# Kernel optimization log

Hardware: AMD Instinct MI355X
Metric: run time of the kernel (lower is better)

Reference implementation:

```python
import jax, jax.numpy as jnp
import numpy as np

N_NODES = 50000
N_EDGES = 800000
IN_FEATS = 128
HEADS = 8
OUT_FEATS = 32
NEG_SLOPE = 0.2


def setup_inputs() -> dict:
    key = jax.random.key(0)
    k_feat, k_w, k_al, k_ar, k_src, k_dst = jax.random.split(key, 6)
    feat = jax.random.normal(k_feat, (N_NODES, IN_FEATS), dtype=jnp.float32)
    W_fc = jax.random.normal(k_w, (HEADS * OUT_FEATS, IN_FEATS), dtype=jnp.float32) * 0.1
    attn_l = jax.random.normal(k_al, (1, HEADS, OUT_FEATS), dtype=jnp.float32) * 0.1
    attn_r = jax.random.normal(k_ar, (1, HEADS, OUT_FEATS), dtype=jnp.float32) * 0.1
    src = jax.random.randint(k_src, (N_EDGES,), 0, N_NODES, dtype=jnp.int32)
    dst = jax.random.randint(k_dst, (N_EDGES,), 0, N_NODES, dtype=jnp.int32)
    return {"feat": feat, "W_fc": W_fc, "attn_l": attn_l, "attn_r": attn_r,
            "src": src, "dst": dst}


def reference(feat, W_fc, attn_l, attn_r, src, dst):
    N = feat.shape[0]
    H, D = attn_l.shape[1], attn_l.shape[2]
    # fc projection: [N, H, D]
    feat_hd = (feat @ W_fc.T).reshape(N, H, D)
    # per-node left/right attention logits: [N, H]
    el = (feat_hd * attn_l).sum(-1)
    er = (feat_hd * attn_r).sum(-1)
    # u_add_v gather -> per-edge score [E, H], then leaky relu
    e = el[src] + er[dst]
    e = jnp.where(e > 0, e, NEG_SLOPE * e)
    # edge softmax: segment softmax over edges grouped by dst node
    m = jax.ops.segment_max(e, dst, num_segments=N)        # [N, H]
    a = jnp.exp(e - m[dst])                                # [E, H]
    z = jax.ops.segment_sum(a, dst, num_segments=N)        # [N, H]
    a = a / z[dst]
    # u_mul_e + sum: weighted scatter-aggregation -> [N, H, D]
    msg = feat_hd[src] * a[:, :, None]                     # [E, H, D]
    out = jax.ops.segment_sum(msg, dst, num_segments=N)
    return out
```

## Files before the change

### kernel.cpp

```cpp
#include <hip/hip_runtime.h>

#define N_NODES_C 50000
#define N_EDGES_C 800000
#define IN_FEATS_C 128
#define HEADS_C 8
#define HD_C 256
#define NEG_SLOPE_C 0.2f
#define SCAN_NBLK 49
#define LDT 136

#define GEMM_BLOCKS 782
#define DEG_BLOCKS 242
#define K1_GRID (GEMM_BLOCKS + DEG_BLOCKS)

typedef __attribute__((ext_vector_type(8))) short bf16x8;
typedef __attribute__((ext_vector_type(4))) float floatx4;

__device__ inline unsigned short f2bf(float f) {
  unsigned int u = __float_as_uint(f);
  unsigned int r = (u + 0x7FFFu + ((u >> 16) & 1u)) >> 16;
  return (unsigned short)r;
}
__device__ inline float bf2f(unsigned short s) {
  unsigned int u = ((unsigned int)s) << 16;
  return __uint_as_float(u);
}

__device__ inline void boff_scan(const int* __restrict__ bsum, int* sboff) {
  int t = threadIdx.x;
  if (t < 64) {
    int own = (t < SCAN_NBLK) ? bsum[t] : 0;
    int v = own;
#pragma unroll
    for (int off = 1; off < 64; off <<= 1) {
      int u = __shfl_up(v, off);
      if (t >= off) v += u;
    }
    sboff[t] = v - own;
  }
  __syncthreads();
}

__global__ __launch_bounds__(256) void front_kernel(
    const float* __restrict__ feat, const float* __restrict__ W,
    const float* __restrict__ attn_l, const float* __restrict__ attn_r,
    const int* __restrict__ dst,
    unsigned short* __restrict__ feat_hd_bf,
    float* __restrict__ el, float* __restrict__ er,
    int* __restrict__ deg) {
  __shared__ __align__(16) unsigned short sA[128 * LDT];
  __shared__ float sAttnL[128];
  __shared__ float sAttnR[128];
  const int bid = blockIdx.x;
  const int t = threadIdx.x;

  if (bid >= GEMM_BLOCKS) {
    for (int e = (bid - GEMM_BLOCKS) * 256 + t; e < N_EDGES_C;
         e += DEG_BLOCKS * 256)
      atomicAdd(&deg[dst[e]], 1);
    return;
  }

  const int nt = bid & 1;
  const int mt = bid >> 1;
  const int m0 = mt * 128;
  const int n0 = nt * 128;

  if (t < 128) {
    sAttnL[t] = attn_l[n0 + t];
    sAttnR[t] = attn_r[n0 + t];
  }
#pragma unroll
  for (int i = 0; i < 16; ++i) {
    int idx = t + i * 256;
    int row = idx >> 5;
    int c4 = idx & 31;
    int gn = m0 + row;
    float4 v = (gn < N_NODES_C)
                   ? *(const float4*)&feat[(size_t)gn * IN_FEATS_C + c4 * 4]
                   : make_float4(0.f, 0.f, 0.f, 0.f);
    ushort4 b;
    b.x = f2bf(v.x); b.y = f2bf(v.y); b.z = f2bf(v.z); b.w = f2bf(v.w);
    *(ushort4*)&sA[row * LDT + c4 * 4] = b;
  }
  __syncthreads();

  const int wid = t >> 6;
  const int lane = t & 63;
  const int quad = lane >> 4;
  const int l16 = lane & 15;
  const int wm = (wid & 1) * 64;
  const int wn = (wid >> 1) * 64;

  floatx4 acc[4][4];
#pragma unroll
  for (int i = 0; i < 4; ++i)
#pragma unroll
    for (int j = 0; j < 4; ++j) acc[i][j] = (floatx4){0.f, 0.f, 0.f, 0.f};

#pragma unroll
  for (int ks = 0; ks < 4; ++ks) {
    int k0 = ks * 32 + quad * 8;
    bf16x8 bfv[4];
#pragma unroll
    for (int n2 = 0; n2 < 4; ++n2) {
      const float* wp = &W[(size_t)(n0 + wn + n2 * 16 + l16) * IN_FEATS_C + k0];
      float4 w0 = *(const float4*)wp;
      float4 w1 = *(const float4*)(wp + 4);
      bf16x8 b;
      b[0] = (short)f2bf(w0.x); b[1] = (short)f2bf(w0.y);
      b[2] = (short)f2bf(w0.z); b[3] = (short)f2bf(w0.w);
      b[4] = (short)f2bf(w1.x); b[5] = (short)f2bf(w1.y);
      b[6] = (short)f2bf(w1.z); b[7] = (short)f2bf(w1.w);
      bfv[n2] = b;
    }
    bf16x8 af[4];
#pragma unroll
    for (int m2 = 0; m2 < 4; ++m2)
      af[m2] = *(const bf16x8*)&sA[(wm + m2 * 16 + l16) * LDT + k0];
#pragma unroll
    for (int m2 = 0; m2 < 4; ++m2)
#pragma unroll
      for (int n2 = 0; n2 < 4; ++n2)
        acc[m2][n2] = __builtin_amdgcn_mfma_f32_16x16x32_bf16(
            af[m2], bfv[n2], acc[m2][n2], 0, 0, 0);
  }
  __syncthreads();

#pragma unroll
  for (int m2 = 0; m2 < 4; ++m2)
#pragma unroll
    for (int n2 = 0; n2 < 4; ++n2)
#pragma unroll
      for (int r = 0; r < 4; ++r) {
        int row = wm + m2 * 16 + quad * 4 + r;
        int col = wn + n2 * 16 + l16;
        sA[row * LDT + col] = f2bf(acc[m2][n2][r]);
      }
  __syncthreads();

#pragma unroll
  for (int i = 0; i < 8; ++i) {
    int idx = t + i * 256;
    int row = idx >> 4;
    int ch = idx & 15;
    int gn = m0 + row;
    if (gn < N_NODES_C) {
      *(uint4*)&feat_hd_bf[(size_t)gn * HD_C + n0 + ch * 8] =
          *(const uint4*)&sA[row * LDT + ch * 8];
    }
  }

  {
    int row = t >> 1;
    int hh = t & 1;
    int gn = m0 + row;
    if (gn < N_NODES_C) {
      const unsigned short* pr = &sA[row * LDT + hh * 64];
      const float* al = &sAttnL[hh * 64];
      const float* ar = &sAttnR[hh * 64];
      float el0 = 0.f, el1 = 0.f, er0 = 0.f, er1 = 0.f;
#pragma unroll
      for (int d = 0; d < 32; ++d) {
        float v0 = bf2f(pr[d]);
        float v1 = bf2f(pr[32 + d]);
        el0 = fmaf(v0, al[d], el0);
        er0 = fmaf(v0, ar[d], er0);
        el1 = fmaf(v1, al[32 + d], el1);
        er1 = fmaf(v1, ar[32 + d], er1);
      }
      int gh = nt * 4 + hh * 2;
      el[gn * HEADS_C + gh + 0] = el0;
      el[gn * HEADS_C + gh + 1] = el1;
      er[gn * HEADS_C + gh + 0] = er0;
      er[gn * HEADS_C + gh + 1] = er1;
    }
  }
}

__global__ __launch_bounds__(256) void scan1_kernel(
    const int* __restrict__ deg, int* __restrict__ row_start,
    int* __restrict__ bsum) {
  __shared__ int s[256];
  int b = blockIdx.x, t = threadIdx.x;
  int i0 = b * 1024 + t * 4;
  int d0 = 0, d1 = 0, d2 = 0, d3 = 0;
  if (i0 + 4 <= N_NODES_C) {
    int4 d = *(const int4*)&deg[i0];
    d0 = d.x; d1 = d.y; d2 = d.z; d3 = d.w;
  } else {
    if (i0 + 0 < N_NODES_C) d0 = deg[i0 + 0];
    if (i0 + 1 < N_NODES_C) d1 = deg[i0 + 1];
    if (i0 + 2 < N_NODES_C) d2 = deg[i0 + 2];
    if (i0 + 3 < N_NODES_C) d3 = deg[i0 + 3];
  }
  int l1 = d0, l2 = l1 + d1, l3 = l2 + d2, l4 = l3 + d3;
  s[t] = l4;
  __syncthreads();
#pragma unroll
  for (int off = 1; off < 256; off <<= 1) {
    int add = (t >= off) ? s[t - off] : 0;
    __syncthreads();
    s[t] += add;
    __syncthreads();
  }
  int excl = s[t] - l4;
  if (i0 + 0 < N_NODES_C) row_start[i0 + 0] = excl + l1;
  if (i0 + 1 < N_NODES_C) row_start[i0 + 1] = excl + l2;
  if (i0 + 2 < N_NODES_C) row_start[i0 + 2] = excl + l3;
  if (i0 + 3 < N_NODES_C) row_start[i0 + 3] = excl + l4;
  if (t == 255) bsum[b] = s[255];
}

__global__ __launch_bounds__(256) void scatter_kernel(
    const int* __restrict__ src, const int* __restrict__ dst,
    const int* __restrict__ row_start, const int* __restrict__ deg,
    const int* __restrict__ bsum, int* __restrict__ cursor,
    int* __restrict__ csr_src) {
  __shared__ int sboff[64];
  boff_scan(bsum, sboff);
  int e = blockIdx.x * 256 + threadIdx.x;
  if (e >= N_EDGES_C) return;
  int d = dst[e];
  int rsf = row_start[d] - deg[d] + sboff[d >> 10];
  int pos = rsf + atomicAdd(&cursor[d], 1);
  csr_src[pos] = src[e];
}

__global__ __launch_bounds__(256) void agg_csr_kernel(
    const unsigned short* __restrict__ feat_hd_bf, const float* __restrict__ el,
    const float* __restrict__ er, const int* __restrict__ row_start,
    const int* __restrict__ deg, const int* __restrict__ bsum,
    const int* __restrict__ csr_src, float* __restrict__ out) {
  __shared__ int sboff[64];
  boff_scan(bsum, sboff);
  int gid = blockIdx.x * 256 + threadIdx.x;
  int node = gid >> 6;
  int lane = threadIdx.x & 63;
  if (node >= N_NODES_C) return;
  int h = lane >> 3;
  int hbase = lane & 56;
  int c = lane * 4;
  float er_d = er[node * HEADS_C + h];
  int dg = deg[node];
  int rs = row_start[node] - dg + sboff[node >> 10];
  float4 acc = make_float4(0.f, 0.f, 0.f, 0.f);
  float zsum = 0.f;

  int i = 0;
  for (; i + 8 <= dg; i += 8) {
    int smine = csr_src[rs + i + (lane & 7)];
    float x = el[smine * HEADS_C + h] + er_d;
    x = x > 0.f ? x : NEG_SLOPE_C * x;
    float w = __expf(x);
    int s0 = csr_src[rs + i + 0];
    int s1 = csr_src[rs + i + 1];
    int s2 = csr_src[rs + i + 2];
    int s3 = csr_src[rs + i + 3];
    int s4 = csr_src[rs + i + 4];
    int s5 = csr_src[rs + i + 5];
    int s6 = csr_src[rs + i + 6];
    int s7 = csr_src[rs + i + 7];
    ushort4 f0 = *(const ushort4*)&feat_hd_bf[(size_t)s0 * HD_C + c];
    ushort4 f1 = *(const ushort4*)&feat_hd_bf[(size_t)s1 * HD_C + c];
    ushort4 f2 = *(const ushort4*)&feat_hd_bf[(size_t)s2 * HD_C + c];
    ushort4 f3 = *(const ushort4*)&feat_hd_bf[(size_t)s3 * HD_C + c];
    ushort4 f4 = *(const ushort4*)&feat_hd_bf[(size_t)s4 * HD_C + c];
    ushort4 f5 = *(const ushort4*)&feat_hd_bf[(size_t)s5 * HD_C + c];
    ushort4 f6 = *(const ushort4*)&feat_hd_bf[(size_t)s6 * HD_C + c];
    ushort4 f7 = *(const ushort4*)&feat_hd_bf[(size_t)s7 * HD_C + c];
    float w0 = __shfl(w, hbase + 0);
    float w1 = __shfl(w, hbase + 1);
    float w2 = __shfl(w, hbase + 2);
    float w3 = __shfl(w, hbase + 3);
    float w4 = __shfl(w, hbase + 4);
    float w5 = __shfl(w, hbase + 5);
    float w6 = __shfl(w, hbase + 6);
    float w7 = __shfl(w, hbase + 7);
    zsum += ((w0 + w1) + (w2 + w3)) + ((w4 + w5) + (w6 + w7));
    acc.x = fmaf(w0, bf2f(f0.x), acc.x); acc.y = fmaf(w0, bf2f(f0.y), acc.y);
    acc.z = fmaf(w0, bf2f(f0.z), acc.z); acc.w = fmaf(w0, bf2f(f0.w), acc.w);
    acc.x = fmaf(w1, bf2f(f1.x), acc.x); acc.y = fmaf(w1, bf2f(f1.y), acc.y);
    acc.z = fmaf(w1, bf2f(f1.z), acc.z); acc.w = fmaf(w1, bf2f(f1.w), acc.w);
    acc.x = fmaf(w2, bf2f(f2.x), acc.x); acc.y = fmaf(w2, bf2f(f2.y), acc.y);
    acc.z = fmaf(w2, bf2f(f2.z), acc.z); acc.w = fmaf(w2, bf2f(f2.w), acc.w);
    acc.x = fmaf(w3, bf2f(f3.x), acc.x); acc.y = fmaf(w3, bf2f(f3.y), acc.y);
    acc.z = fmaf(w3, bf2f(f3.z), acc.z); acc.w = fmaf(w3, bf2f(f3.w), acc.w);
    acc.x = fmaf(w4, bf2f(f4.x), acc.x); acc.y = fmaf(w4, bf2f(f4.y), acc.y);
    acc.z = fmaf(w4, bf2f(f4.z), acc.z); acc.w = fmaf(w4, bf2f(f4.w), acc.w);
    acc.x = fmaf(w5, bf2f(f5.x), acc.x); acc.y = fmaf(w5, bf2f(f5.y), acc.y);
    acc.z = fmaf(w5, bf2f(f5.z), acc.z); acc.w = fmaf(w5, bf2f(f5.w), acc.w);
    acc.x = fmaf(w6, bf2f(f6.x), acc.x); acc.y = fmaf(w6, bf2f(f6.y), acc.y);
    acc.z = fmaf(w6, bf2f(f6.z), acc.z); acc.w = fmaf(w6, bf2f(f6.w), acc.w);
    acc.x = fmaf(w7, bf2f(f7.x), acc.x); acc.y = fmaf(w7, bf2f(f7.y), acc.y);
    acc.z = fmaf(w7, bf2f(f7.z), acc.z); acc.w = fmaf(w7, bf2f(f7.w), acc.w);
  }
  for (; i < dg; ++i) {
    int s = csr_src[rs + i];
    float x = el[s * HEADS_C + h] + er_d;
    x = x > 0.f ? x : NEG_SLOPE_C * x;
    float w = __expf(x);
    zsum += w;
    ushort4 f = *(const ushort4*)&feat_hd_bf[(size_t)s * HD_C + c];
    acc.x = fmaf(w, bf2f(f.x), acc.x);
    acc.y = fmaf(w, bf2f(f.y), acc.y);
    acc.z = fmaf(w, bf2f(f.z), acc.z);
    acc.w = fmaf(w, bf2f(f.w), acc.w);
  }

  float inv = (dg > 0) ? 1.f / zsum : 0.f;
  acc.x *= inv; acc.y *= inv; acc.z *= inv; acc.w *= inv;
  *(float4*)&out[(size_t)node * HD_C + c] = acc;
}

extern "C" void kernel_launch(void* const* d_in, const int* in_sizes, int n_in,
                              void* d_out, int out_size, void* d_ws, size_t ws_size,
                              hipStream_t stream) {
  const float* feat   = (const float*)d_in[0];
  const float* W      = (const float*)d_in[1];
  const float* attn_l = (const float*)d_in[2];
  const float* attn_r = (const float*)d_in[3];
  const int* src      = (const int*)d_in[4];
  const int* dst      = (const int*)d_in[5];
  float* out = (float*)d_out;

  char* ws = (char*)d_ws;
  unsigned short* feat_hd_bf = (unsigned short*)ws;  ws += (size_t)N_NODES_C * HD_C * 2;
  float* el      = (float*)ws;                       ws += (size_t)N_NODES_C * HEADS_C * 4;
  float* er      = (float*)ws;                       ws += (size_t)N_NODES_C * HEADS_C * 4;
  int* deg       = (int*)ws;                         ws += (size_t)N_NODES_C * 4;
  int* cursor    = (int*)ws;                         ws += (size_t)N_NODES_C * 4;
  int* row_start = (int*)ws;                         ws += (size_t)N_NODES_C * 4;
  int* bsum      = (int*)ws;                         ws += 64 * 4;
  int* csr_src   = (int*)ws;                         ws += (size_t)N_EDGES_C * 4;

  hipMemsetAsync(deg, 0, (size_t)N_NODES_C * 2 * 4, stream);

  front_kernel<<<K1_GRID, 256, 0, stream>>>(feat, W, attn_l, attn_r, dst,
                                            feat_hd_bf, el, er, deg);

  scan1_kernel<<<SCAN_NBLK, 256, 0, stream>>>(deg, row_start, bsum);

  scatter_kernel<<<(N_EDGES_C + 255) / 256, 256, 0, stream>>>(
      src, dst, row_start, deg, bsum, cursor, csr_src);

  agg_csr_kernel<<<(N_NODES_C + 3) / 4, 256, 0, stream>>>(
      feat_hd_bf, el, er, row_start, deg, bsum, csr_src, out);
}
```

Before: 259.0 us.

## Reuse degree-count atomic rank for CSR scatter and pipeline neighbor index loads

The degree-counting atomics now record each edge's return value as a per-edge rank, so the scatter kernel computes its CSR slot directly instead of running a second atomic pass over a cursor array. This removes the cursor array and its memset, at the cost of writing and reading an extra 800K-int rank buffer. The aggregation loop is also restructured: each lane loads one neighbor index, the indices are broadcast with shuffles instead of eight redundant global loads, the next block's indices are prefetched, and the tail is handled by masking weights to zero rather than by a scalar remainder loop.

```diff
diff --git a/kernel.cpp b/kernel.cpp
--- a/kernel.cpp
+++ b/kernel.cpp
@@ -47,7 +47,7 @@
     const int* __restrict__ dst,
     unsigned short* __restrict__ feat_hd_bf,
     float* __restrict__ el, float* __restrict__ er,
-    int* __restrict__ deg) {
+    int* __restrict__ deg, int* __restrict__ rank) {
   __shared__ __align__(16) unsigned short sA[128 * LDT];
   __shared__ float sAttnL[128];
   __shared__ float sAttnR[128];
@@ -57,7 +57,7 @@
   if (bid >= GEMM_BLOCKS) {
     for (int e = (bid - GEMM_BLOCKS) * 256 + t; e < N_EDGES_C;
          e += DEG_BLOCKS * 256)
-      atomicAdd(&deg[dst[e]], 1);
+      rank[e] = atomicAdd(&deg[dst[e]], 1);
     return;
   }
 
@@ -215,15 +215,14 @@
 __global__ __launch_bounds__(256) void scatter_kernel(
     const int* __restrict__ src, const int* __restrict__ dst,
     const int* __restrict__ row_start, const int* __restrict__ deg,
-    const int* __restrict__ bsum, int* __restrict__ cursor,
+    const int* __restrict__ bsum, const int* __restrict__ rank,
     int* __restrict__ csr_src) {
   __shared__ int sboff[64];
   boff_scan(bsum, sboff);
   int e = blockIdx.x * 256 + threadIdx.x;
   if (e >= N_EDGES_C) return;
   int d = dst[e];
-  int rsf = row_start[d] - deg[d] + sboff[d >> 10];
-  int pos = rsf + atomicAdd(&cursor[d], 1);
+  int pos = row_start[d] - deg[d] + sboff[d >> 10] + rank[e];
   csr_src[pos] = src[e];
 }
 
@@ -239,6 +238,7 @@
   int lane = threadIdx.x & 63;
   if (node >= N_NODES_C) return;
   int h = lane >> 3;
+  int j8 = lane & 7;
   int hbase = lane & 56;
   int c = lane * 4;
   float er_d = er[node * HEADS_C + h];
@@ -247,65 +247,35 @@
   float4 acc = make_float4(0.f, 0.f, 0.f, 0.f);
   float zsum = 0.f;
 
-  int i = 0;
-  for (; i + 8 <= dg; i += 8) {
-    int smine = csr_src[rs + i + (lane & 7)];
-    float x = el[smine * HEADS_C + h] + er_d;
-    x = x > 0.f ? x : NEG_SLOPE_C * x;
-    float w = __expf(x);
-    int s0 = csr_src[rs + i + 0];
-    int s1 = csr_src[rs + i + 1];
-    int s2 = csr_src[rs + i + 2];
-    int s3 = csr_src[rs + i + 3];
-    int s4 = csr_src[rs + i + 4];
-    int s5 = csr_src[rs + i + 5];
-    int s6 = csr_src[rs + i + 6];
-    int s7 = csr_src[rs + i + 7];
-    ushort4 f0 = *(const ushort4*)&feat_hd_bf[(size_t)s0 * HD_C + c];
-    ushort4 f1 = *(const ushort4*)&feat_hd_bf[(size_t)s1 * HD_C + c];
-    ushort4 f2 = *(const ushort4*)&feat_hd_bf[(size_t)s2 * HD_C + c];
-    ushort4 f3 = *(const ushort4*)&feat_hd_bf[(size_t)s3 * HD_C + c];
-    ushort4 f4 = *(const ushort4*)&feat_hd_bf[(size_t)s4 * HD_C + c];
-    ushort4 f5 = *(const ushort4*)&feat_hd_bf[(size_t)s5 * HD_C + c];
-    ushort4 f6 = *(const ushort4*)&feat_hd_bf[(size_t)s6 * HD_C + c];
-    ushort4 f7 = *(const ushort4*)&feat_hd_bf[(size_t)s7 * HD_C + c];
-    float w0 = __shfl(w, hbase + 0);
-    float w1 = __shfl(w, hbase + 1);
-    float w2 = __shfl(w, hbase + 2);
-    float w3 = __shfl(w, hbase + 3);
-    float w4 = __shfl(w, hbase + 4);
-    float w5 = __shfl(w, hbase + 5);
-    float w6 = __shfl(w, hbase + 6);
-    float w7 = __shfl(w, hbase + 7);
-    zsum += ((w0 + w1) + (w2 + w3)) + ((w4 + w5) + (w6 + w7));
-    acc.x = fmaf(w0, bf2f(f0.x), acc.x); acc.y = fmaf(w0, bf2f(f0.y), acc.y);
-    acc.z = fmaf(w0, bf2f(f0.z), acc.z); acc.w = fmaf(w0, bf2f(f0.w), acc.w);
-    acc.x = fmaf(w1, bf2f(f1.x), acc.x); acc.y = fmaf(w1, bf2f(f1.y), acc.y);
-    acc.z = fmaf(w1, bf2f(f1.z), acc.z); acc.w = fmaf(w1, bf2f(f1.w), acc.w);
-    acc.x = fmaf(w2, bf2f(f2.x), acc.x); acc.y = fmaf(w2, bf2f(f2.y), acc.y);
-    acc.z = fmaf(w2, bf2f(f2.z), acc.z); acc.w = fmaf(w2, bf2f(f2.w), acc.w);
-    acc.x = fmaf(w3, bf2f(f3.x), acc.x); acc.y = fmaf(w3, bf2f(f3.y), acc.y);
-    acc.z = fmaf(w3, bf2f(f3.z), acc.z); acc.w = fmaf(w3, bf2f(f3.w), acc.w);
-    acc.x = fmaf(w4, bf2f(f4.x), acc.x); acc.y = fmaf(w4, bf2f(f4.y), acc.y);
-    acc.z = fmaf(w4, bf2f(f4.z), acc.z); acc.w = fmaf(w4, bf2f(f4.w), acc.w);
-    acc.x = fmaf(w5, bf2f(f5.x), acc.x); acc.y = fmaf(w5, bf2f(f5.y), acc.y);
-    acc.z = fmaf(w5, bf2f(f5.z), acc.z); acc.w = fmaf(w5, bf2f(f5.w), acc.w);
-    acc.x = fmaf(w6, bf2f(f6.x), acc.x); acc.y = fmaf(w6, bf2f(f6.y), acc.y);
-    acc.z = fmaf(w6, bf2f(f6.z), acc.z); acc.w = fmaf(w6, bf2f(f6.w), acc.w);
-    acc.x = fmaf(w7, bf2f(f7.x), acc.x); acc.y = fmaf(w7, bf2f(f7.y), acc.y);
-    acc.z = fmaf(w7, bf2f(f7.z), acc.z); acc.w = fmaf(w7, bf2f(f7.w), acc.w);
-  }
-  for (; i < dg; ++i) {
-    int s = csr_src[rs + i];
-    float x = el[s * HEADS_C + h] + er_d;
-    x = x > 0.f ? x : NEG_SLOPE_C * x;
-    float w = __expf(x);
-    zsum += w;
-    ushort4 f = *(const ushort4*)&feat_hd_bf[(size_t)s * HD_C + c];
-    acc.x = fmaf(w, bf2f(f.x), acc.x);
-    acc.y = fmaf(w, bf2f(f.y), acc.y);
-    acc.z = fmaf(w, bf2f(f.z), acc.z);
-    acc.w = fmaf(w, bf2f(f.w), acc.w);
+  int nb = (dg + 7) >> 3;
+  if (nb > 0) {
+    int myidx = csr_src[rs + min(j8, dg - 1)];
+    for (int b = 0; b < nb; ++b) {
+      int e0 = b * 8;
+      ushort4 f[8];
+#pragma unroll
+      for (int j = 0; j < 8; ++j) {
+        int sj = __shfl(myidx, j);
+        f[j] = *(const ushort4*)&feat_hd_bf[(size_t)sj * HD_C + c];
+      }
+      float x = el[myidx * HEADS_C + h] + er_d;
+      x = x > 0.f ? x : NEG_SLOPE_C * x;
+      float wv = (e0 + j8 < dg) ? __expf(x) : 0.f;
+      int nidx = csr_src[rs + min(e0 + 8 + j8, dg - 1)];
+      float wj[8];
+#pragma unroll
+      for (int j = 0; j < 8; ++j) wj[j] = __shfl(wv, hbase + j);
+      zsum += ((wj[0] + wj[1]) + (wj[2] + wj[3])) +
+              ((wj[4] + wj[5]) + (wj[6] + wj[7]));
+#pragma unroll
+      for (int j = 0; j < 8; ++j) {
+        acc.x = fmaf(wj[j], bf2f(f[j].x), acc.x);
+        acc.y = fmaf(wj[j], bf2f(f[j].y), acc.y);
+        acc.z = fmaf(wj[j], bf2f(f[j].z), acc.z);
+        acc.w = fmaf(wj[j], bf2f(f[j].w), acc.w);
+      }
+      myidx = nidx;
+    }
   }
 
   float inv = (dg > 0) ? 1.f / zsum : 0.f;
@@ -329,20 +299,20 @@
   float* el      = (float*)ws;                       ws += (size_t)N_NODES_C * HEADS_C * 4;
   float* er      = (float*)ws;                       ws += (size_t)N_NODES_C * HEADS_C * 4;
   int* deg       = (int*)ws;                         ws += (size_t)N_NODES_C * 4;
-  int* cursor    = (int*)ws;                         ws += (size_t)N_NODES_C * 4;
   int* row_start = (int*)ws;                         ws += (size_t)N_NODES_C * 4;
   int* bsum      = (int*)ws;                         ws += 64 * 4;
   int* csr_src   = (int*)ws;                         ws += (size_t)N_EDGES_C * 4;
-
-  hipMemsetAsync(deg, 0, (size_t)N_NODES_C * 2 * 4, stream);
+  int* rank      = (int*)ws;                         ws += (size_t)N_EDGES_C * 4;
+
+  hipMemsetAsync(deg, 0, (size_t)N_NODES_C * 4, stream);
 
   front_kernel<<<K1_GRID, 256, 0, stream>>>(feat, W, attn_l, attn_r, dst,
-                                            feat_hd_bf, el, er, deg);
+                                            feat_hd_bf, el, er, deg, rank);
 
   scan1_kernel<<<SCAN_NBLK, 256, 0, stream>>>(deg, row_start, bsum);
 
   scatter_kernel<<<(N_EDGES_C + 255) / 256, 256, 0, stream>>>(
-      src, dst, row_start, deg, bsum, cursor, csr_src);
+      src, dst, row_start, deg, bsum, rank, csr_src);
 
   agg_csr_kernel<<<(N_NODES_C + 3) / 4, 256, 0, stream>>>(
       feat_hd_bf, el, er, row_start, deg, bsum, csr_src, out);
```

New measurement: 226.7 us. -12.5%, faster.
